# Performance work log

Measured on AMD Instinct MI355X. Metric: run time of the kernel, lower is better.

The kernel has to match this reference:

```python
import jax, jax.numpy as jnp
import numpy as np

B, L, D, H, NL = 2, 2048, 1024, 8, 2
HD = D // H
EPS = 1e-8


def layernorm(x, g, b):
    m = jnp.mean(x, axis=-1, keepdims=True)
    v = jnp.mean((x - m) ** 2, axis=-1, keepdims=True)
    return (x - m) / jnp.sqrt(v + EPS) * g + b


def rope(x):
    # x: [B, H, L, HD]; interleaved even/odd rotation as in the torch module
    Ls, Dh = x.shape[-2], x.shape[-1]
    pos = jnp.arange(Ls, dtype=jnp.float32)
    freqs = 1.0 / (10000.0 ** (jnp.arange(0, Dh, 2, dtype=jnp.float32) / Dh))
    ang = pos[:, None] * freqs[None, :]  # [L, HD/2]
    sin, cos = jnp.sin(ang), jnp.cos(ang)
    x1, x2 = x[..., ::2], x[..., 1::2]
    r1 = x1 * cos - x2 * sin
    r2 = x1 * sin + x2 * cos
    return jnp.stack([r1, r2], axis=-1).reshape(x.shape)


def setup_inputs() -> dict:
    key = jax.random.key(0)
    ks = jax.random.split(key, 16)
    s = 0.02

    def w(k, shape):
        return jax.random.normal(k, shape, dtype=jnp.float32) * s

    inp = {
        'seqs': jax.random.normal(ks[0], (B, L, D), dtype=jnp.float32),
        'attn_mask': jnp.broadcast_to(jnp.tril(jnp.ones((L, L), dtype=bool)), (B, L, L)),
        'Wq': w(ks[1], (NL, D, D)), 'bq': jnp.zeros((NL, D), jnp.float32),
        'Wk': w(ks[2], (NL, D, D)), 'bk': jnp.zeros((NL, D), jnp.float32),
        'Wu': w(ks[3], (NL, D, D)), 'bu': jnp.zeros((NL, D), jnp.float32),
        'Wv': w(ks[4], (NL, D, D)), 'bv': jnp.zeros((NL, D), jnp.float32),
        'Wo': w(ks[5], (NL, D, D)), 'bo': jnp.zeros((NL, D), jnp.float32),
        'W1': w(ks[6], (NL, D, D)), 'b1': jnp.zeros((NL, D), jnp.float32),
        'W2': w(ks[7], (NL, D, D)), 'b2': jnp.zeros((NL, D), jnp.float32),
        'ln1_g': jnp.ones((NL, D), jnp.float32), 'ln1_b': jnp.zeros((NL, D), jnp.float32),
        'ln2_g': jnp.ones((NL, D), jnp.float32), 'ln2_b': jnp.zeros((NL, D), jnp.float32),
        'lnf_g': jnp.ones((D,), jnp.float32), 'lnf_b': jnp.zeros((D,), jnp.float32),
    }
    return inp


def reference(seqs, attn_mask, Wq, bq, Wk, bk, Wu, bu, Wv, bv, Wo, bo,
              W1, b1, W2, b2, ln1_g, ln1_b, ln2_g, ln2_b, lnf_g, lnf_b):
    x = seqs
    Bsz, Ls, Dm = x.shape
    mask4 = attn_mask[:, None, :, :]  # [B,1,L,L]
    for i in range(NL):
        h = layernorm(x, ln1_g[i], ln1_b[i])

        def proj(Wm, bm):
            t = jnp.einsum('bld,od->blo', h, Wm) + bm
            return t.reshape(Bsz, Ls, H, HD).transpose(0, 2, 1, 3)

        Q = rope(proj(Wq[i], bq[i]))
        K = rope(proj(Wk[i], bk[i]))
        U = proj(Wu[i], bu[i])
        V = proj(Wv[i], bv[i])
        scores = jnp.einsum('bhqd,bhkd->bhqk', Q, K) / jnp.sqrt(jnp.float32(HD))
        scores = jnp.where(mask4, scores, jnp.float32(-1e9))
        wts = jax.nn.silu(scores)  # SiLU replaces softmax (HSTU)
        a = jnp.einsum('bhqk,bhkd->bhqd', wts, V) * U  # U-gated output
        a = a.transpose(0, 2, 1, 3).reshape(Bsz, Ls, Dm)
        a = jnp.einsum('bld,od->blo', a, Wo[i]) + bo[i]
        x = x + a
        h2 = layernorm(x, ln2_g[i], ln2_b[i])
        p = jnp.einsum('bld,od->blo', h2, W1[i]) + b1[i]
        f = jnp.einsum('bld,od->blo', p * jax.nn.silu(p), W2[i]) + b2[i]  # SwiGLU-style
        x = x + f
    return layernorm(x, lnf_g, lnf_b)
```

## Files before the change

### kernel.cpp

```cpp
#include <hip/hip_runtime.h>
#include <stdint.h>

typedef __attribute__((ext_vector_type(4))) float f32x4;
typedef __attribute__((ext_vector_type(16))) float f32x16;
typedef __attribute__((ext_vector_type(8))) short s16x8;
typedef __attribute__((ext_vector_type(4))) unsigned int u32x4;

#define D_ 1024
#define LQ 2048
#define HH_ 8
#define HD_ 128

static __device__ __forceinline__ float bf2f(ushort u){
  union { unsigned int i; float f; } v; v.i = ((unsigned int)u) << 16; return v.f;
}
static __device__ __forceinline__ ushort f2bf(float f){
  union { float f; unsigned int i; } v; v.f = f;
  unsigned int r = v.i + 0x7fffu + ((v.i >> 16) & 1u);
  return (ushort)(r >> 16);
}
static __device__ __forceinline__ unsigned int pkbf(float lo, float hi){
  unsigned int r;
  asm("v_cvt_pk_bf16_f32 %0, %1, %2" : "=v"(r) : "v"(lo), "v"(hi));
  return r;
}

struct WP { const float* s[7]; };
__global__ __launch_bounds__(256) void convert_weights(WP wp, ushort* __restrict__ dst){
  int w = blockIdx.x >> 7, blk = blockIdx.x & 127, t = threadIdx.x;
  const float4* s = (const float4*)wp.s[w];
  ushort4* d = (ushort4*)(dst + (size_t)w * 1048576);
  int base = blk * 2048 + t;
  #pragma unroll
  for (int r = 0; r < 8; r++){
    float4 v = s[base + r * 256];
    ushort4 o; o.x = f2bf(v.x); o.y = f2bf(v.y); o.z = f2bf(v.z); o.w = f2bf(v.w);
    d[base + r * 256] = o;
  }
}

template<int OUTF>
__global__ __launch_bounds__(256) void ln_kernel(const float* __restrict__ x,
    const float* __restrict__ g, const float* __restrict__ bb,
    float* __restrict__ outf, ushort* __restrict__ outb){
  int row = blockIdx.x, t = threadIdx.x;
  const float4* xr = (const float4*)(x + (size_t)row * D_);
  float4 v = xr[t];
  float s = v.x + v.y + v.z + v.w;
  float sq = v.x*v.x + v.y*v.y + v.z*v.z + v.w*v.w;
  #pragma unroll
  for (int o = 32; o; o >>= 1){ s += __shfl_down(s, o, 64); sq += __shfl_down(sq, o, 64); }
  __shared__ float red[8];
  int lane = t & 63, wv = t >> 6;
  if (!lane){ red[wv] = s; red[wv + 4] = sq; }
  __syncthreads();
  float S = red[0] + red[1] + red[2] + red[3];
  float SQ = red[4] + red[5] + red[6] + red[7];
  float m = S * (1.f / 1024.f);
  float var = SQ * (1.f / 1024.f) - m * m;
  float inv = rsqrtf(var + 1e-8f);
  float4 gv = ((const float4*)g)[t], bv = ((const float4*)bb)[t];
  float4 y;
  y.x = (v.x - m) * inv * gv.x + bv.x;
  y.y = (v.y - m) * inv * gv.y + bv.y;
  y.z = (v.z - m) * inv * gv.z + bv.z;
  y.w = (v.w - m) * inv * gv.w + bv.w;
  if (OUTF){
    ((float4*)outf)[(size_t)row * 256 + t] = y;
  } else {
    ushort4 o4; o4.x = f2bf(y.x); o4.y = f2bf(y.y); o4.z = f2bf(y.z); o4.w = f2bf(y.w);
    ((ushort4*)outb)[(size_t)row * 256 + t] = o4;
  }
}

struct P4 { ushort* d[4]; const float* b[4]; };

__global__ __launch_bounds__(512, 2) void gemm_qkuv(
    const ushort* __restrict__ A, const ushort* __restrict__ W, P4 io){
  __shared__ ushort As[3][256 * 64];
  __shared__ ushort Bs[3][128 * 64];
  int bid = (blockIdx.x & 7) * 64 + (blockIdx.x >> 3);
  int m0 = (bid >> 5) << 8;
  int n0g = (bid & 31) << 7;
  int t = threadIdx.x, lane = t & 63, wv = t >> 6;
  int l15 = lane & 15, quad = lane >> 4;
  int wm4 = (wv & 3) << 6;
  int wn2 = (wv >> 2) << 6;

  auto STAGE = [&](int buf, int kt){
    int k0 = kt << 6;
    #pragma unroll
    for (int r = 0; r < 4; r++){
      int g = r * 512 + (wv << 6);
      int gl = g + lane;
      int row = gl >> 3;
      int kk = ((gl & 7) ^ (row & 7)) << 3;
      __builtin_amdgcn_global_load_lds(
          (const __attribute__((address_space(1))) unsigned int*)(A + (size_t)(m0 + row) * 1024 + k0 + kk),
          (__attribute__((address_space(3))) unsigned int*)&As[buf][g * 8], 16, 0, 0);
    }
    #pragma unroll
    for (int r = 0; r < 2; r++){
      int g = r * 512 + (wv << 6);
      int gl = g + lane;
      int row = gl >> 3;
      int kk = ((gl & 7) ^ (row & 7)) << 3;
      __builtin_amdgcn_global_load_lds(
          (const __attribute__((address_space(1))) unsigned int*)(W + (size_t)(n0g + row) * 1024 + k0 + kk),
          (__attribute__((address_space(3))) unsigned int*)&Bs[buf][g * 8], 16, 0, 0);
    }
  };

  f32x4 acc[4][4] = {};
  STAGE(0, 0);
  STAGE(1, 1);
  int bc = 0, bs = 2;
  for (int kt = 0; kt < 16; kt++){
    if (kt < 15) asm volatile("s_waitcnt vmcnt(6)" ::: "memory");
    else         asm volatile("s_waitcnt vmcnt(0)" ::: "memory");
    __builtin_amdgcn_s_barrier();
    asm volatile("" ::: "memory");
    __builtin_amdgcn_sched_barrier(0);
    if (kt + 2 < 16) STAGE(bs, kt + 2);
    const ushort* Ab = &As[bc][0];
    const ushort* Bb = &Bs[bc][0];
    s16x8 afr[4][2];
    #pragma unroll
    for (int mi = 0; mi < 4; mi++)
      #pragma unroll
      for (int kd = 0; kd < 2; kd++){
        int R = wm4 + mi * 16 + l15;
        afr[mi][kd] = *(const s16x8*)&Ab[R * 64 + (((kd << 2) | quad) ^ (R & 7)) * 8];
      }
    s16x8 bfr[2][2];
    #pragma unroll
    for (int ni = 0; ni < 2; ni++)
      #pragma unroll
      for (int kd = 0; kd < 2; kd++){
        int R = wn2 + ni * 16 + l15;
        bfr[ni][kd] = *(const s16x8*)&Bb[R * 64 + (((kd << 2) | quad) ^ (R & 7)) * 8];
      }
    __builtin_amdgcn_s_setprio(1);
    #pragma unroll
    for (int kd = 0; kd < 2; kd++)
      #pragma unroll
      for (int mi = 0; mi < 4; mi++)
        #pragma unroll
        for (int ni = 0; ni < 2; ni++)
          acc[mi][ni] = __builtin_amdgcn_mfma_f32_16x16x32_bf16(afr[mi][kd], bfr[ni][kd], acc[mi][ni], 0, 0, 0);
    __builtin_amdgcn_s_setprio(0);
    s16x8 bfr2[2][2];
    #pragma unroll
    for (int ni = 0; ni < 2; ni++)
      #pragma unroll
      for (int kd = 0; kd < 2; kd++){
        int R = wn2 + (ni + 2) * 16 + l15;
        bfr2[ni][kd] = *(const s16x8*)&Bb[R * 64 + (((kd << 2) | quad) ^ (R & 7)) * 8];
      }
    __builtin_amdgcn_s_setprio(1);
    #pragma unroll
    for (int kd = 0; kd < 2; kd++)
      #pragma unroll
      for (int mi = 0; mi < 4; mi++)
        #pragma unroll
        for (int ni = 0; ni < 2; ni++)
          acc[mi][ni + 2] = __builtin_amdgcn_mfma_f32_16x16x32_bf16(afr[mi][kd], bfr2[ni][kd], acc[mi][ni + 2], 0, 0, 0);
    __builtin_amdgcn_s_setprio(0);
    bc = (bc == 2) ? 0 : bc + 1;
    bs = (bs == 2) ? 0 : bs + 1;
  }
  int sel = n0g >> 10;
  ushort* dst = io.d[sel];
  const float* bias = io.b[sel];
  int ncol = n0g & 1023;
  #pragma unroll
  for (int mi = 0; mi < 4; mi++){
    int gm = m0 + wm4 + mi * 16 + quad * 4;
    #pragma unroll
    for (int ni = 0; ni < 4; ni++){
      int cn = ncol + wn2 + ni * 16 + l15;
      float bv = bias[cn];
      if (sel < 2){
        int i2 = (cn & 127) >> 1;
        float freq = __builtin_amdgcn_exp2f(-0.20762050f * (float)i2);
        int odd = cn & 1;
        #pragma unroll
        for (int r = 0; r < 4; r++){
          float val = acc[mi][ni][r] + bv;
          float pv = __shfl_xor(val, 1, 64);
          int pos = (gm + r) & 2047;
          float ang = (float)pos * freq;
          float sv, cv; __sincosf(ang, &sv, &cv);
          float res = odd ? (pv * sv + val * cv) : (val * cv - pv * sv);
          dst[(size_t)(gm + r) * 1024 + cn] = f2bf(res);
        }
      } else {
        #pragma unroll
        for (int r = 0; r < 4; r++){
          float val = acc[mi][ni][r] + bv;
          dst[(size_t)(gm + r) * 1024 + cn] = f2bf(val);
        }
      }
    }
  }
}

template<int EPI>
__global__ __launch_bounds__(256, 2) void gemm_k2(
    const ushort* __restrict__ A, const ushort* __restrict__ W,
    const float* __restrict__ bias, ushort* __restrict__ dst,
    const float* __restrict__ resid, float* __restrict__ outf){
  __shared__ ushort As[64 * 64];
  __shared__ ushort Bs[128 * 64];
  int m0 = (blockIdx.x >> 3) << 6;
  int n0 = (blockIdx.x & 7) << 7;
  int t = threadIdx.x, lane = t & 63, wv = t >> 6;
  int l15 = lane & 15, quad = lane >> 4;
  int wm = (wv & 1) << 5, wn = (wv >> 1) << 6;
  f32x4 acc[2][4] = {};
  for (int k0 = 0; k0 < 1024; k0 += 64){
    #pragma unroll
    for (int r = 0; r < 6; r++){
      int cb = (r < 2 ? r * 256 : (r - 2) * 256) + wv * 64;
      int c = cb + lane;
      int row = c >> 3, j = c & 7;
      int kk = ((j ^ (row & 7)) << 3);
      if (r < 2){
        __builtin_amdgcn_global_load_lds(
            (const __attribute__((address_space(1))) unsigned int*)(A + (size_t)(m0 + row) * 1024 + k0 + kk),
            (__attribute__((address_space(3))) unsigned int*)&As[cb * 8], 16, 0, 0);
      } else {
        __builtin_amdgcn_global_load_lds(
            (const __attribute__((address_space(1))) unsigned int*)(W + (size_t)(n0 + row) * 1024 + k0 + kk),
            (__attribute__((address_space(3))) unsigned int*)&Bs[cb * 8], 16, 0, 0);
      }
    }
    __syncthreads();
    #pragma unroll
    for (int kd = 0; kd < 2; kd++){
      s16x8 afr[2], bfr[4];
      #pragma unroll
      for (int mi = 0; mi < 2; mi++){
        int R = wm + mi * 16 + l15;
        afr[mi] = *(const s16x8*)&As[R * 64 + (((kd << 2) | quad) ^ (R & 7)) * 8];
      }
      #pragma unroll
      for (int ni = 0; ni < 4; ni++){
        int R = wn + ni * 16 + l15;
        bfr[ni] = *(const s16x8*)&Bs[R * 64 + (((kd << 2) | quad) ^ (R & 7)) * 8];
      }
      #pragma unroll
      for (int mi = 0; mi < 2; mi++)
        #pragma unroll
        for (int ni = 0; ni < 4; ni++)
          acc[mi][ni] = __builtin_amdgcn_mfma_f32_16x16x32_bf16(afr[mi], bfr[ni], acc[mi][ni], 0, 0, 0);
    }
    __syncthreads();
  }
  #pragma unroll
  for (int mi = 0; mi < 2; mi++){
    int gm = m0 + wm + mi * 16 + quad * 4;
    #pragma unroll
    for (int ni = 0; ni < 4; ni++){
      int cn = n0 + wn + ni * 16 + l15;
      float bv = bias[cn];
      #pragma unroll
      for (int r = 0; r < 4; r++){
        float val = acc[mi][ni][r] + bv;
        size_t o = (size_t)(gm + r) * 1024 + cn;
        if (EPI == 1){ outf[o] = resid[o] + val; }
        else {
          float sg = __builtin_amdgcn_rcpf(1.f + __expf(-val));
          dst[o] = f2bf(val * val * sg);
        }
      }
    }
  }
}

__global__ __launch_bounds__(256) void transpose_v(const ushort* __restrict__ Vb, ushort* __restrict__ Vt){
  int bidx = blockIdx.x;
  int dt = bidx & 1, lt = (bidx >> 1) & 31, bh = bidx >> 6;
  int b = bh >> 3, hh = bh & 7;
  int l0 = lt << 6, d0 = dt << 6;
  __shared__ ushort tile[64][66];
  int t = threadIdx.x;
  #pragma unroll
  for (int r = 0; r < 8; r++){
    int idx = r * 256 + t;
    int row = idx >> 5, cu = idx & 31;
    unsigned int val = *(const unsigned int*)(Vb + (size_t)(b * LQ + l0 + row) * D_ + hh * HD_ + d0 + cu * 2);
    *(unsigned int*)&tile[row][cu * 2] = val;
  }
  __syncthreads();
  #pragma unroll
  for (int r = 0; r < 8; r++){
    int idx = r * 256 + t;
    int drow = idx >> 5, lu = idx & 31;
    unsigned int val = (unsigned int)tile[lu * 2][drow] | ((unsigned int)tile[lu * 2 + 1][drow] << 16);
    int kk = lu * 2;
    int x = kk & 15;
    int kkp = (kk & 48) | ((x & 4) << 1) | ((x & 8) >> 1) | (x & 3);
    *(unsigned int*)(Vt + ((size_t)(bh * HD_ + d0 + drow)) * LQ + l0 + kkp) = val;
  }
}

__global__ __launch_bounds__(256, 2) void attn_kernel(
    const ushort* __restrict__ Q, const ushort* __restrict__ K,
    const ushort* __restrict__ Vt,
    ushort* __restrict__ Po0, ushort* __restrict__ Po1){
  __shared__ ushort Ks[2][64 * 128];
  __shared__ ushort Vs[2][128 * 64];
  int t = threadIdx.x, lane = t & 63, wv = t >> 6;
  int l31 = lane & 31, h = lane >> 5;
  int idx = blockIdx.x;
  int bh = idx & 15;
  int s = idx >> 4;
  int qt = (s < 16) ? (15 - (s >> 1)) : ((s - 16) >> 1);
  int half = s & 1;
  int ntiles = 2 * qt + 2;
  int c0 = qt + 1;
  int klo = half ? c0 : 0;
  int khi = half ? ntiles : c0;
  if (klo >= khi) return;
  int b = bh >> 3, hh = bh & 7;
  int q0 = qt << 7;
  const float scale = 0.08838834764831845f;

  s16x8 qf[8];
  const ushort* qbase = Q + (size_t)(b * LQ + q0 + (wv << 5) + l31) * D_ + hh * HD_;
  #pragma unroll
  for (int kd = 0; kd < 8; kd++) qf[kd] = *(const s16x8*)(qbase + kd * 16 + h * 8);

  auto STAGE = [&](int p, int kt){
    int k0 = kt << 6;
    #pragma unroll
    for (int r = 0; r < 4; r++){
      int cb = r * 256 + (wv << 6);
      int c = cb + lane;
      int R = c >> 4, sl = c & 15;
      int gg = sl ^ (R & 7);
      __builtin_amdgcn_global_load_lds(
          (const __attribute__((address_space(1))) unsigned int*)(K + (size_t)(b * LQ + k0 + R) * D_ + hh * HD_ + gg * 8),
          (__attribute__((address_space(3))) unsigned int*)&Ks[p][cb * 8], 16, 0, 0);
    }
    #pragma unroll
    for (int r = 0; r < 4; r++){
      int cb = r * 256 + (wv << 6);
      int c = cb + lane;
      int R = c >> 3, sl = c & 7;
      int gg = sl ^ (R & 7);
      __builtin_amdgcn_global_load_lds(
          (const __attribute__((address_space(1))) unsigned int*)(Vt + (size_t)(bh * HD_ + R) * LQ + k0 + gg * 8),
          (__attribute__((address_space(3))) unsigned int*)&Vs[p][cb * 8], 16, 0, 0);
    }
  };

  f32x16 acc_o[4] = {};
  int qg = q0 + (wv << 5) + l31;

  STAGE(0, klo);
  __syncthreads();
  for (int kt = klo; kt < khi; kt++){
    int p = (kt - klo) & 1;
    if (kt + 1 < khi) STAGE(p ^ 1, kt + 1);
    f32x16 sacc[2] = {};
    #pragma unroll
    for (int kd = 0; kd < 8; kd++){
      #pragma unroll
      for (int kb = 0; kb < 2; kb++){
        int R = (kb << 5) + l31;
        s16x8 af = *(const s16x8*)&Ks[p][(R * 16 + (((kd << 1) | h) ^ (R & 7))) * 8];
        sacc[kb] = __builtin_amdgcn_mfma_f32_32x32x16_bf16(af, qf[kd], sacc[kb], 0, 0, 0);
      }
    }
    int k0 = kt << 6;
    s16x8 pf[4];
    #pragma unroll
    for (int kb = 0; kb < 2; kb++){
      float pvv[16];
      #pragma unroll
      for (int r = 0; r < 16; r++){
        int kg = k0 + (kb << 5) + (r & 3) + ((r >> 2) << 3) + (h << 2);
        float sv = sacc[kb][r] * scale;
        float pp = sv * __builtin_amdgcn_rcpf(1.f + __expf(-sv));
        pvv[r] = (kg <= qg) ? pp : 0.f;
      }
      #pragma unroll
      for (int cc = 0; cc < 2; cc++){
        union { u32x4 u; s16x8 v; } w;
        w.u[0] = pkbf(pvv[cc*8+0], pvv[cc*8+1]);
        w.u[1] = pkbf(pvv[cc*8+2], pvv[cc*8+3]);
        w.u[2] = pkbf(pvv[cc*8+4], pvv[cc*8+5]);
        w.u[3] = pkbf(pvv[cc*8+6], pvv[cc*8+7]);
        pf[(kb << 1) | cc] = w.v;
      }
    }
    #pragma unroll
    for (int kv = 0; kv < 4; kv++){
      #pragma unroll
      for (int nt = 0; nt < 4; nt++){
        int R = (nt << 5) + l31;
        s16x8 vf = *(const s16x8*)&Vs[p][(R * 8 + (((kv << 1) | h) ^ (R & 7))) * 8];
        acc_o[nt] = __builtin_amdgcn_mfma_f32_32x32x16_bf16(pf[kv], vf, acc_o[nt], 0, 0, 0);
      }
    }
    __syncthreads();
  }
  ushort* Po = half ? Po1 : Po0;
  #pragma unroll
  for (int nt = 0; nt < 4; nt++){
    #pragma unroll
    for (int r = 0; r < 16; r++){
      int qq = q0 + (wv << 5) + (r & 3) + ((r >> 2) << 3) + (h << 2);
      int dd = (nt << 5) + l31;
      Po[(size_t)(b * LQ + qq) * D_ + hh * HD_ + dd] = f2bf(acc_o[nt][r]);
    }
  }
}

__global__ __launch_bounds__(256) void attn_reduce(
    const ushort* __restrict__ Po0, const ushort* __restrict__ Po1,
    const ushort* __restrict__ U, ushort* __restrict__ Aout){
  int i = (blockIdx.x * 256 + threadIdx.x) * 4;
  ushort4 p0 = *(const ushort4*)(Po0 + i);
  ushort4 p1 = *(const ushort4*)(Po1 + i);
  float v0 = bf2f(p0.x) + bf2f(p1.x);
  float v1 = bf2f(p0.y) + bf2f(p1.y);
  float v2 = bf2f(p0.z) + bf2f(p1.z);
  float v3 = bf2f(p0.w) + bf2f(p1.w);
  ushort4 u = *(const ushort4*)(U + i);
  ushort4 o;
  o.x = f2bf(v0 * bf2f(u.x)); o.y = f2bf(v1 * bf2f(u.y));
  o.z = f2bf(v2 * bf2f(u.z)); o.w = f2bf(v3 * bf2f(u.w));
  *(ushort4*)(Aout + i) = o;
}

extern "C" void kernel_launch(void* const* d_in, const int* in_sizes, int n_in,
                              void* d_out, int out_size, void* d_ws, size_t ws_size,
                              hipStream_t stream){
  const float* seqs = (const float*)d_in[0];
  const float* bq = (const float*)d_in[3];
  const float* bk = (const float*)d_in[5];
  const float* bu = (const float*)d_in[7];
  const float* bv = (const float*)d_in[9];
  const float* bo = (const float*)d_in[11];
  const float* b1 = (const float*)d_in[13];
  const float* b2 = (const float*)d_in[15];
  const float* ln1g = (const float*)d_in[16];
  const float* ln1b = (const float*)d_in[17];
  const float* ln2g = (const float*)d_in[18];
  const float* ln2b = (const float*)d_in[19];
  const float* lnfg = (const float*)d_in[20];
  const float* lnfb = (const float*)d_in[21];

  char* base = (char*)d_ws;
  const size_t MB = 1u << 20;
  if (ws_size < 78 * MB) return;
  ushort* wbf = (ushort*)base;
  ushort* h   = (ushort*)(base + 14 * MB);
  ushort* Qb  = (ushort*)(base + 22 * MB);
  ushort* Kb  = (ushort*)(base + 30 * MB);
  ushort* Ub  = (ushort*)(base + 38 * MB);
  ushort* Vb  = (ushort*)(base + 46 * MB);
  ushort* Vt  = (ushort*)(base + 54 * MB);
  float*  xb  = (float*)(base + 62 * MB);
  ushort* ab  = h;

  const size_t DD = 1048576;
  for (int i = 0; i < 2; i++){
    WP wp;
    for (int j = 0; j < 7; j++)
      wp.s[j] = (const float*)d_in[2 + 2 * j] + (size_t)i * DD;
    convert_weights<<<7 * 128, 256, 0, stream>>>(wp, wbf);
    const ushort* Wl = wbf;
    const float* xin = (i == 0) ? seqs : xb;
    ln_kernel<0><<<4096, 256, 0, stream>>>(xin, ln1g + i * D_, ln1b + i * D_, nullptr, h);
    P4 io_qkuv = {{Qb, Kb, Ub, Vb}, {bq + i * D_, bk + i * D_, bu + i * D_, bv + i * D_}};
    gemm_qkuv<<<512, 512, 0, stream>>>(h, Wl, io_qkuv);
    transpose_v<<<1024, 256, 0, stream>>>(Vb, Vt);
    attn_kernel<<<512, 256, 0, stream>>>(Qb, Kb, Vt, ab, Vb);
    attn_reduce<<<4096, 256, 0, stream>>>(ab, Vb, Ub, ab);
    gemm_k2<1><<<512, 256, 0, stream>>>(ab, Wl + 4 * DD, bo + i * D_, nullptr, xin, xb);
    ln_kernel<0><<<4096, 256, 0, stream>>>(xb, ln2g + i * D_, ln2b + i * D_, nullptr, h);
    gemm_k2<2><<<512, 256, 0, stream>>>(h, Wl + 5 * DD, b1 + i * D_, Qb, nullptr, nullptr);
    gemm_k2<1><<<512, 256, 0, stream>>>(Qb, Wl + 6 * DD, b2 + i * D_, nullptr, xb, xb);
  }
  ln_kernel<1><<<4096, 256, 0, stream>>>(xb, lnfg, lnfb, (float*)d_out, nullptr);
}
```

Baseline: 506.1 us.

## Enlarge QKUV GEMM tile to 256x256 with ping-pong LDS schedule

Rewrites the fused QKUV projection GEMM to use 256x256 output tiles per block instead of 256x128, halving the grid to 256 blocks, with a new XCD-aware tile mapping. Staging moves to a double-buffered scheme with split A/B halves, and the k-loop is interleaved: fragment loads, global-to-LDS copies and MFMA quarter-blocks are separated by barriers and waitcnts. The aim is more reuse per loaded tile and less global traffic. The cost is twice the accumulator registers and many more barriers, and a grid of 256 blocks may leave CUs idle.

After: 487.2 us. 1.04x faster.

```diff
diff --git a/kernel.cpp b/kernel.cpp
--- a/kernel.cpp
+++ b/kernel.cpp
@@ -77,69 +77,80 @@
 
 __global__ __launch_bounds__(512, 2) void gemm_qkuv(
     const ushort* __restrict__ A, const ushort* __restrict__ W, P4 io){
-  __shared__ ushort As[3][256 * 64];
-  __shared__ ushort Bs[3][128 * 64];
-  int bid = (blockIdx.x & 7) * 64 + (blockIdx.x >> 3);
-  int m0 = (bid >> 5) << 8;
-  int n0g = (bid & 31) << 7;
+  __shared__ ushort As[2][2][128 * 64];
+  __shared__ ushort Bs[2][2][128 * 64];
+  int xcd = blockIdx.x & 7, slot = blockIdx.x >> 3;
+  int mip = (xcd >> 1) * 4 + (slot >> 3);
+  int nip = (xcd & 1) * 8 + (slot & 7);
+  int m0 = mip << 8, n0 = nip << 8;
   int t = threadIdx.x, lane = t & 63, wv = t >> 6;
   int l15 = lane & 15, quad = lane >> 4;
-  int wm4 = (wv & 3) << 6;
-  int wn2 = (wv >> 2) << 6;
-
-  auto STAGE = [&](int buf, int kt){
-    int k0 = kt << 6;
-    #pragma unroll
-    for (int r = 0; r < 4; r++){
-      int g = r * 512 + (wv << 6);
-      int gl = g + lane;
-      int row = gl >> 3;
-      int kk = ((gl & 7) ^ (row & 7)) << 3;
+  int wm = wv >> 2;
+  int wn = wv & 3;
+  int bh = wn >> 1;
+  int bcol = (wn & 1) << 6;
+
+  const ushort* Ab0 = &As[0][wm][0];
+  const ushort* Ab1 = &As[1][wm][0];
+  const ushort* Bb0 = &Bs[0][bh][0];
+  const ushort* Bb1 = &Bs[1][bh][0];
+
+  auto stA = [&](int buf, int half, int kt){
+    #pragma unroll
+    for (int i = 0; i < 2; i++){
+      int gb = i * 512 + (wv << 6);
+      int g = gb + lane;
+      int row = g >> 3;
+      int kk = ((g & 7) ^ (row & 7)) << 3;
       __builtin_amdgcn_global_load_lds(
-          (const __attribute__((address_space(1))) unsigned int*)(A + (size_t)(m0 + row) * 1024 + k0 + kk),
-          (__attribute__((address_space(3))) unsigned int*)&As[buf][g * 8], 16, 0, 0);
-    }
-    #pragma unroll
-    for (int r = 0; r < 2; r++){
-      int g = r * 512 + (wv << 6);
-      int gl = g + lane;
-      int row = gl >> 3;
-      int kk = ((gl & 7) ^ (row & 7)) << 3;
+          (const __attribute__((address_space(1))) unsigned int*)(A + (size_t)(m0 + half * 128 + row) * 1024 + kt * 64 + kk),
+          (__attribute__((address_space(3))) unsigned int*)&As[buf][half][gb * 8], 16, 0, 0);
+    }
+  };
+  auto stB = [&](int buf, int half, int kt){
+    #pragma unroll
+    for (int i = 0; i < 2; i++){
+      int gb = i * 512 + (wv << 6);
+      int g = gb + lane;
+      int row = g >> 3;
+      int kk = ((g & 7) ^ (row & 7)) << 3;
       __builtin_amdgcn_global_load_lds(
-          (const __attribute__((address_space(1))) unsigned int*)(W + (size_t)(n0g + row) * 1024 + k0 + kk),
-          (__attribute__((address_space(3))) unsigned int*)&Bs[buf][g * 8], 16, 0, 0);
-    }
-  };
-
-  f32x4 acc[4][4] = {};
-  STAGE(0, 0);
-  STAGE(1, 1);
-  int bc = 0, bs = 2;
-  for (int kt = 0; kt < 16; kt++){
-    if (kt < 15) asm volatile("s_waitcnt vmcnt(6)" ::: "memory");
-    else         asm volatile("s_waitcnt vmcnt(0)" ::: "memory");
-    __builtin_amdgcn_s_barrier();
-    asm volatile("" ::: "memory");
-    __builtin_amdgcn_sched_barrier(0);
-    if (kt + 2 < 16) STAGE(bs, kt + 2);
-    const ushort* Ab = &As[bc][0];
-    const ushort* Bb = &Bs[bc][0];
-    s16x8 afr[4][2];
+          (const __attribute__((address_space(1))) unsigned int*)(W + (size_t)(n0 + half * 128 + row) * 1024 + kt * 64 + kk),
+          (__attribute__((address_space(3))) unsigned int*)&Bs[buf][half][gb * 8], 16, 0, 0);
+    }
+  };
+
+  f32x4 acc[8][4] = {};
+  s16x8 afr[4][2], bfrL[2][2], bfrH[2][2];
+
+  auto dsA = [&](const ushort* base, int mq){
     #pragma unroll
     for (int mi = 0; mi < 4; mi++)
       #pragma unroll
       for (int kd = 0; kd < 2; kd++){
-        int R = wm4 + mi * 16 + l15;
-        afr[mi][kd] = *(const s16x8*)&Ab[R * 64 + (((kd << 2) | quad) ^ (R & 7)) * 8];
-      }
-    s16x8 bfr[2][2];
+        int R = mq * 64 + mi * 16 + l15;
+        afr[mi][kd] = *(const s16x8*)&base[R * 64 + (((kd << 2) | quad) ^ (R & 7)) * 8];
+      }
+  };
+  auto dsBL = [&](const ushort* base){
     #pragma unroll
     for (int ni = 0; ni < 2; ni++)
       #pragma unroll
       for (int kd = 0; kd < 2; kd++){
-        int R = wn2 + ni * 16 + l15;
-        bfr[ni][kd] = *(const s16x8*)&Bb[R * 64 + (((kd << 2) | quad) ^ (R & 7)) * 8];
-      }
+        int r = bcol + ni * 16 + l15;
+        bfrL[ni][kd] = *(const s16x8*)&base[r * 64 + (((kd << 2) | quad) ^ (r & 7)) * 8];
+      }
+  };
+  auto dsBH = [&](const ushort* base){
+    #pragma unroll
+    for (int ni = 0; ni < 2; ni++)
+      #pragma unroll
+      for (int kd = 0; kd < 2; kd++){
+        int r = bcol + 32 + ni * 16 + l15;
+        bfrH[ni][kd] = *(const s16x8*)&base[r * 64 + (((kd << 2) | quad) ^ (r & 7)) * 8];
+      }
+  };
+  auto MM = [&](int mq, int nq, s16x8 (&bf)[2][2]){
     __builtin_amdgcn_s_setprio(1);
     #pragma unroll
     for (int kd = 0; kd < 2; kd++)
@@ -147,46 +158,83 @@
       for (int mi = 0; mi < 4; mi++)
         #pragma unroll
         for (int ni = 0; ni < 2; ni++)
-          acc[mi][ni] = __builtin_amdgcn_mfma_f32_16x16x32_bf16(afr[mi][kd], bfr[ni][kd], acc[mi][ni], 0, 0, 0);
+          acc[mq * 4 + mi][nq * 2 + ni] = __builtin_amdgcn_mfma_f32_16x16x32_bf16(
+              afr[mi][kd], bf[ni][kd], acc[mq * 4 + mi][nq * 2 + ni], 0, 0, 0);
     __builtin_amdgcn_s_setprio(0);
-    s16x8 bfr2[2][2];
-    #pragma unroll
-    for (int ni = 0; ni < 2; ni++)
-      #pragma unroll
-      for (int kd = 0; kd < 2; kd++){
-        int R = wn2 + (ni + 2) * 16 + l15;
-        bfr2[ni][kd] = *(const s16x8*)&Bb[R * 64 + (((kd << 2) | quad) ^ (R & 7)) * 8];
-      }
-    __builtin_amdgcn_s_setprio(1);
-    #pragma unroll
-    for (int kd = 0; kd < 2; kd++)
-      #pragma unroll
-      for (int mi = 0; mi < 4; mi++)
-        #pragma unroll
-        for (int ni = 0; ni < 2; ni++)
-          acc[mi][ni + 2] = __builtin_amdgcn_mfma_f32_16x16x32_bf16(afr[mi][kd], bfr2[ni][kd], acc[mi][ni + 2], 0, 0, 0);
-    __builtin_amdgcn_s_setprio(0);
-    bc = (bc == 2) ? 0 : bc + 1;
-    bs = (bs == 2) ? 0 : bs + 1;
-  }
-  int sel = n0g >> 10;
-  ushort* dst = io.d[sel];
-  const float* bias = io.b[sel];
-  int ncol = n0g & 1023;
-  #pragma unroll
-  for (int mi = 0; mi < 4; mi++){
-    int gm = m0 + wm4 + mi * 16 + quad * 4;
-    #pragma unroll
-    for (int ni = 0; ni < 4; ni++){
-      int cn = ncol + wn2 + ni * 16 + l15;
-      float bv = bias[cn];
-      if (sel < 2){
-        int i2 = (cn & 127) >> 1;
-        float freq = __builtin_amdgcn_exp2f(-0.20762050f * (float)i2);
-        int odd = cn & 1;
+  };
+
+  stA(0, 0, 0); stA(0, 1, 0); stB(0, 0, 0); stB(0, 1, 0);
+  stB(1, 0, 1); stB(1, 1, 1); stA(1, 0, 1);
+  asm volatile("s_waitcnt vmcnt(6)" ::: "memory");
+  __builtin_amdgcn_s_barrier();
+
+  for (int it = 0; it < 8; ++it){
+    int kt1 = 2 * it + 1, kt2 = 2 * it + 2, kt3 = 2 * it + 3;
+    bool g1 = (it < 7);
+    dsA(Ab0, 0); dsBL(Bb0);
+    stA(1, 1, kt1);
+    __builtin_amdgcn_s_barrier();
+    asm volatile("s_waitcnt lgkmcnt(0)" ::: "memory");
+    MM(0, 0, bfrL);
+    __builtin_amdgcn_s_barrier();
+    dsBH(Bb0);
+    __builtin_amdgcn_s_barrier();
+    asm volatile("s_waitcnt lgkmcnt(0)" ::: "memory");
+    MM(0, 1, bfrH);
+    __builtin_amdgcn_s_barrier();
+    dsA(Ab0, 1);
+    if (g1) stB(0, 0, kt2);
+    __builtin_amdgcn_s_barrier();
+    asm volatile("s_waitcnt lgkmcnt(0)" ::: "memory");
+    MM(1, 0, bfrL);
+    __builtin_amdgcn_s_barrier();
+    if (g1){ stB(0, 1, kt2); stA(0, 0, kt2); }
+    if (g1) asm volatile("s_waitcnt vmcnt(6)" ::: "memory");
+    else    asm volatile("s_waitcnt vmcnt(0)" ::: "memory");
+    __builtin_amdgcn_s_barrier();
+    MM(1, 1, bfrH);
+    __builtin_amdgcn_s_barrier();
+    dsA(Ab1, 0); dsBL(Bb1);
+    if (g1) stA(0, 1, kt2);
+    __builtin_amdgcn_s_barrier();
+    asm volatile("s_waitcnt lgkmcnt(0)" ::: "memory");
+    MM(0, 0, bfrL);
+    __builtin_amdgcn_s_barrier();
+    dsBH(Bb1);
+    __builtin_amdgcn_s_barrier();
+    asm volatile("s_waitcnt lgkmcnt(0)" ::: "memory");
+    MM(0, 1, bfrH);
+    __builtin_amdgcn_s_barrier();
+    dsA(Ab1, 1);
+    if (g1) stB(1, 0, kt3);
+    __builtin_amdgcn_s_barrier();
+    asm volatile("s_waitcnt lgkmcnt(0)" ::: "memory");
+    MM(1, 0, bfrL);
+    __builtin_amdgcn_s_barrier();
+    if (g1){ stB(1, 1, kt3); stA(1, 0, kt3); }
+    if (g1) asm volatile("s_waitcnt vmcnt(6)" ::: "memory");
+    __builtin_amdgcn_s_barrier();
+    MM(1, 1, bfrH);
+    __builtin_amdgcn_s_barrier();
+  }
+
+  #pragma unroll
+  for (int ni4 = 0; ni4 < 4; ni4++){
+    int cng = n0 + (wn << 6) + ni4 * 16 + l15;
+    int sel = cng >> 10;
+    ushort* dst = io.d[sel];
+    float bv = io.b[sel][cng & 1023];
+    int cn = cng & 1023;
+    if (sel < 2){
+      int i2 = (cn & 127) >> 1;
+      float freq = __builtin_amdgcn_exp2f(-0.20762050f * (float)i2);
+      int odd = cn & 1;
+      #pragma unroll
+      for (int mi8 = 0; mi8 < 8; mi8++){
+        int gm = m0 + (wm << 7) + mi8 * 16 + quad * 4;
         #pragma unroll
         for (int r = 0; r < 4; r++){
-          float val = acc[mi][ni][r] + bv;
+          float val = acc[mi8][ni4][r] + bv;
           float pv = __shfl_xor(val, 1, 64);
           int pos = (gm + r) & 2047;
           float ang = (float)pos * freq;
@@ -194,10 +242,14 @@
           float res = odd ? (pv * sv + val * cv) : (val * cv - pv * sv);
           dst[(size_t)(gm + r) * 1024 + cn] = f2bf(res);
         }
-      } else {
+      }
+    } else {
+      #pragma unroll
+      for (int mi8 = 0; mi8 < 8; mi8++){
+        int gm = m0 + (wm << 7) + mi8 * 16 + quad * 4;
         #pragma unroll
         for (int r = 0; r < 4; r++){
-          float val = acc[mi][ni][r] + bv;
+          float val = acc[mi8][ni4][r] + bv;
           dst[(size_t)(gm + r) * 1024 + cn] = f2bf(val);
         }
       }
@@ -477,7 +529,7 @@
     const float* xin = (i == 0) ? seqs : xb;
     ln_kernel<0><<<4096, 256, 0, stream>>>(xin, ln1g + i * D_, ln1b + i * D_, nullptr, h);
     P4 io_qkuv = {{Qb, Kb, Ub, Vb}, {bq + i * D_, bk + i * D_, bu + i * D_, bv + i * D_}};
-    gemm_qkuv<<<512, 512, 0, stream>>>(h, Wl, io_qkuv);
+    gemm_qkuv<<<256, 512, 0, stream>>>(h, Wl, io_qkuv);
     transpose_v<<<1024, 256, 0, stream>>>(Vb, Vt);
     attn_kernel<<<512, 256, 0, stream>>>(Qb, Kb, Vt, ab, Vb);
     attn_reduce<<<4096, 256, 0, stream>>>(ab, Vb, Ub, ab);
```
